# Kernel tuning notes

Measured on AMD Instinct MI355X. Metric: run time of the kernel, lower is better.

Reference implementation:

```python
import jax, jax.numpy as jnp
import numpy as np

NUM_GROUPS = 4
KERNEL_SIZE = 3


def _conv1x1(x, w, b):
    # x: [B,Cin,H,W], w: [Cout,Cin], b: [Cout]
    return jnp.einsum('bchw,oc->bohw', x, w) + b[None, :, None, None]


def _unfold(t, ks):
    # t: [B,G,Gd,H,W] -> patches [B,G,Gd,ks*ks,H,W] with zero padding (pad=ks//2)
    pad = ks // 2
    H, W = t.shape[-2:]
    tp = jnp.pad(t, ((0, 0), (0, 0), (0, 0), (pad, pad), (pad, pad)))
    return jnp.stack([tp[..., i:i + H, j:j + W]
                      for i in range(ks) for j in range(ks)], axis=3)


def setup_inputs() -> dict:
    key = jax.random.key(0)
    ks = jax.random.split(key, 7)
    B, Cin, C, H, W = 4, 256, 256, 64, 64
    s = 1.0 / np.sqrt(Cin)
    return {
        'x': jax.random.normal(ks[0], (B, Cin, H, W), dtype=jnp.float32),
        'wq': jax.random.normal(ks[1], (C, Cin), dtype=jnp.float32) * s,
        'bq': jax.random.normal(ks[2], (C,), dtype=jnp.float32) * 0.01,
        'wk': jax.random.normal(ks[3], (C, Cin), dtype=jnp.float32) * s,
        'bk': jax.random.normal(ks[4], (C,), dtype=jnp.float32) * 0.01,
        'wv': jax.random.normal(ks[5], (C, Cin), dtype=jnp.float32) * s,
        'bv': jax.random.normal(ks[6], (C,), dtype=jnp.float32) * 0.01,
    }


def reference(x, wq, bq, wk, bk, wv, bv):
    B, _, H, W = x.shape
    C = wq.shape[0]
    G = NUM_GROUPS
    Gd = C // G
    q = _conv1x1(x, wq, bq).reshape(B, G, Gd, H, W)
    k = _conv1x1(x, wk, bk).reshape(B, G, Gd, H, W)
    v = _conv1x1(x, wv, bv).reshape(B, G, Gd, H, W)
    kp = _unfold(k, KERNEL_SIZE)  # [B,G,Gd,k2,H,W]
    vp = _unfold(v, KERNEL_SIZE)  # [B,G,Gd,k2,H,W]
    attn = jnp.einsum('bgdhw,bgdphw->bgphw', q, kp)  # [B,G,k2,H,W]
    attn = jax.nn.softmax(attn, axis=2)
    out = jnp.einsum('bgphw,bgdphw->bgdhw', attn, vp)  # [B,G,Gd,H,W]
    return out.reshape(B, C, H, W)
```

## Files before the change

kernel.cpp:

```cpp
#include <hip/hip_runtime.h>
#include <cstddef>
#include <cstdint>

#define BDIM 4
#define HH   64
#define WW   64
#define HWSZ 4096
#define CIN  256

typedef __attribute__((ext_vector_type(4))) float f32x4;
typedef _Float16 f16x4_t __attribute__((ext_vector_type(4)));
typedef _Float16 f16x8_t __attribute__((ext_vector_type(8)));

__device__ __forceinline__ void lds_load16(const void* g, void* l) {
    __builtin_amdgcn_global_load_lds(
        (const __attribute__((address_space(1))) unsigned int*)g,
        (__attribute__((address_space(3))) unsigned int*)l, 16, 0, 0);
}

__global__ __launch_bounds__(512, 2) void fused_kernel(
    const float* __restrict__ x,
    const float* __restrict__ wq, const float* __restrict__ bq,
    const float* __restrict__ wk, const float* __restrict__ bk,
    const float* __restrict__ wv, const float* __restrict__ bv,
    float* __restrict__ out)
{
    __shared__ float    As[128 * 32];
    __shared__ float    Bs[32 * 384];
    __shared__ _Float16 qlds[256 * 64];
    __shared__ _Float16 klds[384 * 64];

    const int t   = threadIdx.x;
    const int bx0 = blockIdx.x;
    const int bx  = (bx0 & 7) * 32 + (bx0 >> 3);
    const int g   = bx & 3;
    const int ht  = (bx >> 2) & 15;
    const int b   = bx >> 6;
    const int h0  = ht * 4;

    const int l    = t & 63;
    const int wid  = t >> 6;
    const int lrow = l & 15;
    const int grp  = l >> 4;
    const int grp4 = grp * 4;
    const int wmA  = wid >> 2;
    const int wnA  = wid & 3;

    const float* xb = x + (size_t)b * CIN * HWSZ;

    const int ms  = t >> 3;
    const int kbs = ((t & 7) ^ (ms & 7)) * 4;
    const float* aSrcQ = wq + (size_t)(g * 64 + ms) * CIN + kbs;
    const float* aSrcK = wk + (size_t)(g * 64 + ms) * CIN + kbs;
    const float* aSrcV = wv + (size_t)(g * 64 + ms) * CIN + kbs;

    const float* bSrc[6];
    #pragma unroll
    for (int i = 0; i < 6; ++i) {
        const unsigned U = i * 512 + t;
        const unsigned k = U / 96u;
        const unsigned rem = U - k * 96u;
        const int r  = (int)(rem >> 4);
        const int u0 = (int)(rem & 15);
        int srow = h0 - 1 + r;
        srow = srow < 0 ? 0 : (srow > 63 ? 63 : srow);
        const int cu = u0 ^ (((int)(k >> 3)) << 2);
        bSrc[i] = xb + (size_t)k * HWSZ + srow * 64 + cu * 4;
    }

    const float* biasA = wmA ? bk : bq;
    f32x4 accA[4][6];
    #pragma unroll
    for (int mi = 0; mi < 4; ++mi) {
        const f32x4 bb = *(const f32x4*)&biasA[g * 64 + mi * 16 + grp4];
        #pragma unroll
        for (int ni = 0; ni < 6; ++ni) accA[mi][ni] = bb;
    }

    for (int kt = 0; kt < 8; ++kt) {
        const size_t ko = (size_t)kt * 32;
        lds_load16(aSrcQ + ko, As + t * 4);
        lds_load16(aSrcK + ko, As + 2048 + t * 4);
        #pragma unroll
        for (int i = 0; i < 6; ++i)
            lds_load16(bSrc[i] + ko * HWSZ, Bs + (i * 512 + t) * 4);
        __syncthreads();

        f16x8_t af[4];
        #pragma unroll
        for (int mi = 0; mi < 4; ++mi) {
            const int m = wmA * 64 + mi * 16 + lrow;
            const int s = m & 7;
            const f32x4 a0 = *(const f32x4*)&As[m * 32 + ((2 * grp) ^ s) * 4];
            const f32x4 a1 = *(const f32x4*)&As[m * 32 + ((2 * grp + 1) ^ s) * 4];
            f16x8_t f;
            #pragma unroll
            for (int j = 0; j < 4; ++j) { f[j] = (_Float16)a0[j]; f[4 + j] = (_Float16)a1[j]; }
            af[mi] = f;
        }
        f16x8_t bf[6];
        #pragma unroll
        for (int ni = 0; ni < 6; ++ni) {
            const int px  = wnA * 96 + ni * 16 + lrow;
            const int fo  = ((px >> 2) ^ (grp << 2)) * 4 + (px & 3);
            f16x8_t f;
            #pragma unroll
            for (int j = 0; j < 8; ++j) f[j] = (_Float16)Bs[(grp * 8 + j) * 384 + fo];
            bf[ni] = f;
        }
        #pragma unroll
        for (int mi = 0; mi < 4; ++mi)
            #pragma unroll
            for (int ni = 0; ni < 6; ++ni)
                accA[mi][ni] = __builtin_amdgcn_mfma_f32_16x16x32_f16(
                    af[mi], bf[ni], accA[mi][ni], 0, 0, 0);
        __syncthreads();
    }

    #pragma unroll
    for (int ni = 0; ni < 6; ++ni) {
        const int px = wnA * 96 + ni * 16 + lrow;
        const int spx = (wmA == 0) ? (px - 64) : px;
        const bool ok = (wmA == 0) ? (spx >= 0 && spx < 256) : true;
        _Float16* dl = (wmA == 0) ? qlds : klds;
        #pragma unroll
        for (int mi = 0; mi < 4; ++mi) {
            if (ok) {
                const int cb  = mi * 2 + (grp >> 1);
                const int off = (grp & 1) * 4;
                f16x4_t hv;
                #pragma unroll
                for (int j = 0; j < 4; ++j) hv[j] = (_Float16)accA[mi][ni][j];
                *(f16x4_t*)&dl[spx * 64 + ((cb ^ (spx & 7)) * 8) + off] = hv;
            }
        }
    }
    __syncthreads();

    const int pxi  = wid * 32 + (l & 31);
    const int chh  = l >> 5;
    const int hq   = h0 + (pxi >> 6);
    const int wcol = pxi & 63;

    float qf[32];
    #pragma unroll
    for (int jj = 0; jj < 4; ++jj) {
        const int cb = chh * 4 + jj;
        const f16x8_t qv = *(const f16x8_t*)&qlds[pxi * 64 + ((cb ^ (pxi & 7)) * 8)];
        #pragma unroll
        for (int e = 0; e < 8; ++e) qf[jj * 8 + e] = (float)qv[e];
    }

    float lg[9];
    #pragma unroll
    for (int p = 0; p < 9; ++p) {
        const int dh = p / 3 - 1, dw = p % 3 - 1;
        const int h2 = hq + dh, w2 = wcol + dw;
        float part = 0.f;
        if (h2 >= 0 && h2 < HH && w2 >= 0 && w2 < WW) {
            const int hpx = pxi + 64 + dh * 64 + dw;
            #pragma unroll
            for (int jj = 0; jj < 4; ++jj) {
                const int cb = chh * 4 + jj;
                const f16x8_t kv = *(const f16x8_t*)&klds[hpx * 64 + ((cb ^ (hpx & 7)) * 8)];
                #pragma unroll
                for (int e = 0; e < 8; ++e) part += qf[jj * 8 + e] * (float)kv[e];
            }
        }
        part += __shfl_xor(part, 32, 64);
        lg[p] = part;
    }

    float mx = lg[0];
    #pragma unroll
    for (int p = 1; p < 9; ++p) mx = fmaxf(mx, lg[p]);
    float a[9];
    float sum = 0.f;
    #pragma unroll
    for (int p = 0; p < 9; ++p) { a[p] = __expf(lg[p] - mx); sum += a[p]; }
    const float inv = 1.f / sum;
    #pragma unroll
    for (int p = 0; p < 9; ++p) a[p] *= inv;

    f32x4 accB[4][3];
    #pragma unroll
    for (int mi = 0; mi < 4; ++mi) {
        const f32x4 bb = *(const f32x4*)&bv[g * 64 + mi * 16 + grp4];
        #pragma unroll
        for (int ni = 0; ni < 3; ++ni) accB[mi][ni] = bb;
    }

    for (int kt = 0; kt < 8; ++kt) {
        const size_t ko = (size_t)kt * 32;
        lds_load16(aSrcV + ko, As + t * 4);
        #pragma unroll
        for (int i = 0; i < 6; ++i)
            lds_load16(bSrc[i] + ko * HWSZ, Bs + (i * 512 + t) * 4);
        __syncthreads();

        f16x8_t af[4];
        #pragma unroll
        for (int mi = 0; mi < 4; ++mi) {
            const int m = mi * 16 + lrow;
            const int s = m & 7;
            const f32x4 a0 = *(const f32x4*)&As[m * 32 + ((2 * grp) ^ s) * 4];
            const f32x4 a1 = *(const f32x4*)&As[m * 32 + ((2 * grp + 1) ^ s) * 4];
            f16x8_t f;
            #pragma unroll
            for (int j = 0; j < 4; ++j) { f[j] = (_Float16)a0[j]; f[4 + j] = (_Float16)a1[j]; }
            af[mi] = f;
        }
        f16x8_t bf[3];
        #pragma unroll
        for (int ni = 0; ni < 3; ++ni) {
            const int px = wid * 48 + ni * 16 + lrow;
            const int fo = ((px >> 2) ^ (grp << 2)) * 4 + (px & 3);
            f16x8_t f;
            #pragma unroll
            for (int j = 0; j < 8; ++j) f[j] = (_Float16)Bs[(grp * 8 + j) * 384 + fo];
            bf[ni] = f;
        }
        #pragma unroll
        for (int mi = 0; mi < 4; ++mi)
            #pragma unroll
            for (int ni = 0; ni < 3; ++ni)
                accB[mi][ni] = __builtin_amdgcn_mfma_f32_16x16x32_f16(
                    af[mi], bf[ni], accB[mi][ni], 0, 0, 0);
        __syncthreads();
    }

    #pragma unroll
    for (int ni = 0; ni < 3; ++ni) {
        const int px = wid * 48 + ni * 16 + lrow;
        #pragma unroll
        for (int mi = 0; mi < 4; ++mi) {
            const int cb  = mi * 2 + (grp >> 1);
            const int off = (grp & 1) * 4;
            f16x4_t hv;
            #pragma unroll
            for (int j = 0; j < 4; ++j) hv[j] = (_Float16)accB[mi][ni][j];
            *(f16x4_t*)&klds[px * 64 + ((cb ^ (px & 7)) * 8) + off] = hv;
        }
    }
    __syncthreads();

    float oacc[32];
    #pragma unroll
    for (int c = 0; c < 32; ++c) oacc[c] = 0.f;
    #pragma unroll
    for (int p = 0; p < 9; ++p) {
        const int dh = p / 3 - 1, dw = p % 3 - 1;
        const int h2 = hq + dh, w2 = wcol + dw;
        if (h2 < 0 || h2 >= HH || w2 < 0 || w2 >= WW) continue;
        const float ap = a[p];
        const int hpx = pxi + 64 + dh * 64 + dw;
        #pragma unroll
        for (int jj = 0; jj < 4; ++jj) {
            const int cb = chh * 4 + jj;
            const f16x8_t vv = *(const f16x8_t*)&klds[hpx * 64 + ((cb ^ (hpx & 7)) * 8)];
            #pragma unroll
            for (int e = 0; e < 8; ++e) oacc[jj * 8 + e] += ap * (float)vv[e];
        }
    }

    float* ob = out + ((size_t)(b * 256 + g * 64 + chh * 32)) * HWSZ + ht * 256 + pxi;
    #pragma unroll
    for (int c = 0; c < 32; ++c) ob[(size_t)c * HWSZ] = oacc[c];
}

extern "C" void kernel_launch(void* const* d_in, const int* in_sizes, int n_in,
                              void* d_out, int out_size, void* d_ws, size_t ws_size,
                              hipStream_t stream) {
    const float* x  = (const float*)d_in[0];
    const float* wq = (const float*)d_in[1];
    const float* bq = (const float*)d_in[2];
    const float* wk = (const float*)d_in[3];
    const float* bk = (const float*)d_in[4];
    const float* wv = (const float*)d_in[5];
    const float* bv = (const float*)d_in[6];
    float* out = (float*)d_out;

    fused_kernel<<<dim3(256), 512, 0, stream>>>(x, wq, bq, wk, bk, wv, bv, out);
}
```

Baseline: 37.54 us.

## Halve row tile, stage fp16 operands in LDS, aliased shared memory

Shrinks each block's spatial tile from 4 to 2 image rows, doubling the grid to 512 blocks. Global loads now go through registers and are converted to fp16 once before the LDS store, replacing the async global-to-LDS fp32 copies and their per-read conversions. Shared memory is packed into one aliased buffer so more blocks fit per CU, and launch bounds ask for 4 blocks. The cost is a larger share of halo rows recomputed for K/V (4 rows loaded per 2 output rows) and loads that are no longer asynchronous.

```diff
diff --git a/kernel.cpp b/kernel.cpp
--- a/kernel.cpp
+++ b/kernel.cpp
@@ -1,8 +1,6 @@
 #include <hip/hip_runtime.h>
 #include <cstddef>
-#include <cstdint>
-
-#define BDIM 4
+
 #define HH   64
 #define WW   64
 #define HWSZ 4096
@@ -12,143 +10,131 @@
 typedef _Float16 f16x4_t __attribute__((ext_vector_type(4)));
 typedef _Float16 f16x8_t __attribute__((ext_vector_type(8)));
 
-__device__ __forceinline__ void lds_load16(const void* g, void* l) {
-    __builtin_amdgcn_global_load_lds(
-        (const __attribute__((address_space(1))) unsigned int*)g,
-        (__attribute__((address_space(3))) unsigned int*)l, 16, 0, 0);
-}
-
-__global__ __launch_bounds__(512, 2) void fused_kernel(
+__global__ __launch_bounds__(512, 4) void fused_kernel(
     const float* __restrict__ x,
     const float* __restrict__ wq, const float* __restrict__ bq,
     const float* __restrict__ wk, const float* __restrict__ bk,
     const float* __restrict__ wv, const float* __restrict__ bv,
     float* __restrict__ out)
 {
-    __shared__ float    As[128 * 32];
-    __shared__ float    Bs[32 * 384];
-    __shared__ _Float16 qlds[256 * 64];
-    __shared__ _Float16 klds[384 * 64];
+    __shared__ __align__(16) char smem[57344];
+    _Float16* As   = (_Float16*)smem;
+    _Float16* Bs   = (_Float16*)(smem + 8192);
+    _Float16* qlds = (_Float16*)smem;
+    _Float16* klds = (_Float16*)(smem + 24576);
 
     const int t   = threadIdx.x;
     const int bx0 = blockIdx.x;
-    const int bx  = (bx0 & 7) * 32 + (bx0 >> 3);
+    const int bx  = (bx0 & 7) * 64 + (bx0 >> 3);
     const int g   = bx & 3;
-    const int ht  = (bx >> 2) & 15;
-    const int b   = bx >> 6;
-    const int h0  = ht * 4;
-
-    const int l    = t & 63;
-    const int wid  = t >> 6;
-    const int lrow = l & 15;
-    const int grp  = l >> 4;
+    const int ht  = (bx >> 2) & 31;
+    const int b   = bx >> 7;
+    const int h0  = ht * 2;
+
+    const int l    = t & 63, wid = t >> 6;
+    const int lrow = l & 15, grp = l >> 4;
     const int grp4 = grp * 4;
-    const int wmA  = wid >> 2;
-    const int wnA  = wid & 3;
+    const int swzr = (lrow >> 1) & 3;
+    const int wmA  = wid >> 2, wnA = wid & 3;
 
     const float* xb = x + (size_t)b * CIN * HWSZ;
 
-    const int ms  = t >> 3;
-    const int kbs = ((t & 7) ^ (ms & 7)) * 4;
-    const float* aSrcQ = wq + (size_t)(g * 64 + ms) * CIN + kbs;
-    const float* aSrcK = wk + (size_t)(g * 64 + ms) * CIN + kbs;
-    const float* aSrcV = wv + (size_t)(g * 64 + ms) * CIN + kbs;
-
-    const float* bSrc[6];
-    #pragma unroll
-    for (int i = 0; i < 6; ++i) {
-        const unsigned U = i * 512 + t;
-        const unsigned k = U / 96u;
-        const unsigned rem = U - k * 96u;
-        const int r  = (int)(rem >> 4);
-        const int u0 = (int)(rem & 15);
-        int srow = h0 - 1 + r;
-        srow = srow < 0 ? 0 : (srow > 63 ? 63 : srow);
-        const int cu = u0 ^ (((int)(k >> 3)) << 2);
-        bSrc[i] = xb + (size_t)k * HWSZ + srow * 64 + cu * 4;
-    }
+    const int smA = t >> 2, skA = t & 3;
+    const float* aqk = (smA < 64 ? wq + (size_t)(g * 64 + smA) * CIN
+                                 : wk + (size_t)(g * 64 + smA - 64) * CIN) + skA * 8;
+    const int awz = smA * 32 + ((skA ^ ((smA >> 1) & 3)) << 3);
+
+    const int mv = (t >> 2) & 63;
+    const float* avv = wv + (size_t)(g * 64 + mv) * CIN + skA * 8;
+    const int awzV = mv * 32 + ((skA ^ ((mv >> 1) & 3)) << 3);
+
+    const int spx0 = t & 127, skB = t >> 7;
+    const int spx1 = spx0 + 128;
+    int sr0 = h0 - 1 + (spx0 >> 6); sr0 = sr0 < 0 ? 0 : sr0;
+    int sr1 = h0 - 1 + (spx1 >> 6); sr1 = sr1 > 63 ? 63 : sr1;
+    const float* bgp0 = xb + (size_t)(skB * 8) * HWSZ + sr0 * 64 + (spx0 & 63);
+    const float* bgp1 = xb + (size_t)(skB * 8) * HWSZ + sr1 * 64 + (spx1 & 63);
+    const int bwz0 = spx0 * 32 + ((skB ^ ((spx0 >> 1) & 3)) << 3);
+    const int bwz1 = spx1 * 32 + ((skB ^ ((spx1 >> 1) & 3)) << 3);
 
     const float* biasA = wmA ? bk : bq;
-    f32x4 accA[4][6];
+    f32x4 accA[4][4];
     #pragma unroll
     for (int mi = 0; mi < 4; ++mi) {
         const f32x4 bb = *(const f32x4*)&biasA[g * 64 + mi * 16 + grp4];
         #pragma unroll
-        for (int ni = 0; ni < 6; ++ni) accA[mi][ni] = bb;
+        for (int ni = 0; ni < 4; ++ni) accA[mi][ni] = bb;
     }
 
     for (int kt = 0; kt < 8; ++kt) {
-        const size_t ko = (size_t)kt * 32;
-        lds_load16(aSrcQ + ko, As + t * 4);
-        lds_load16(aSrcK + ko, As + 2048 + t * 4);
-        #pragma unroll
-        for (int i = 0; i < 6; ++i)
-            lds_load16(bSrc[i] + ko * HWSZ, Bs + (i * 512 + t) * 4);
-        __syncthreads();
-
-        f16x8_t af[4];
-        #pragma unroll
-        for (int mi = 0; mi < 4; ++mi) {
-            const int m = wmA * 64 + mi * 16 + lrow;
-            const int s = m & 7;
-            const f32x4 a0 = *(const f32x4*)&As[m * 32 + ((2 * grp) ^ s) * 4];
-            const f32x4 a1 = *(const f32x4*)&As[m * 32 + ((2 * grp + 1) ^ s) * 4];
-            f16x8_t f;
-            #pragma unroll
-            for (int j = 0; j < 4; ++j) { f[j] = (_Float16)a0[j]; f[4 + j] = (_Float16)a1[j]; }
-            af[mi] = f;
-        }
-        f16x8_t bf[6];
-        #pragma unroll
-        for (int ni = 0; ni < 6; ++ni) {
-            const int px  = wnA * 96 + ni * 16 + lrow;
-            const int fo  = ((px >> 2) ^ (grp << 2)) * 4 + (px & 3);
-            f16x8_t f;
-            #pragma unroll
-            for (int j = 0; j < 8; ++j) f[j] = (_Float16)Bs[(grp * 8 + j) * 384 + fo];
-            bf[ni] = f;
-        }
-        #pragma unroll
-        for (int mi = 0; mi < 4; ++mi)
-            #pragma unroll
-            for (int ni = 0; ni < 6; ++ni)
+        const float4 A0 = *(const float4*)(aqk + kt * 32);
+        const float4 A1 = *(const float4*)(aqk + kt * 32 + 4);
+        float lb0[8], lb1[8];
+        #pragma unroll
+        for (int j = 0; j < 8; ++j) lb0[j] = bgp0[(size_t)(kt * 32 + j) * HWSZ];
+        #pragma unroll
+        for (int j = 0; j < 8; ++j) lb1[j] = bgp1[(size_t)(kt * 32 + j) * HWSZ];
+        __syncthreads();
+
+        f16x8_t fa, f0, f1;
+        const float* pA0 = (const float*)&A0;
+        const float* pA1 = (const float*)&A1;
+        #pragma unroll
+        for (int j = 0; j < 4; ++j) { fa[j] = (_Float16)pA0[j]; fa[4 + j] = (_Float16)pA1[j]; }
+        #pragma unroll
+        for (int j = 0; j < 8; ++j) { f0[j] = (_Float16)lb0[j]; f1[j] = (_Float16)lb1[j]; }
+        *(f16x8_t*)&As[awz]  = fa;
+        *(f16x8_t*)&Bs[bwz0] = f0;
+        *(f16x8_t*)&Bs[bwz1] = f1;
+        __syncthreads();
+
+        f16x8_t af[4], bf[4];
+        #pragma unroll
+        for (int mi = 0; mi < 4; ++mi)
+            af[mi] = *(const f16x8_t*)&As[(wmA * 64 + mi * 16 + lrow) * 32 + ((grp ^ swzr) << 3)];
+        #pragma unroll
+        for (int ni = 0; ni < 4; ++ni)
+            bf[ni] = *(const f16x8_t*)&Bs[(wnA * 64 + ni * 16 + lrow) * 32 + ((grp ^ swzr) << 3)];
+        #pragma unroll
+        for (int mi = 0; mi < 4; ++mi)
+            #pragma unroll
+            for (int ni = 0; ni < 4; ++ni)
                 accA[mi][ni] = __builtin_amdgcn_mfma_f32_16x16x32_f16(
                     af[mi], bf[ni], accA[mi][ni], 0, 0, 0);
-        __syncthreads();
-    }
-
-    #pragma unroll
-    for (int ni = 0; ni < 6; ++ni) {
-        const int px = wnA * 96 + ni * 16 + lrow;
-        const int spx = (wmA == 0) ? (px - 64) : px;
-        const bool ok = (wmA == 0) ? (spx >= 0 && spx < 256) : true;
-        _Float16* dl = (wmA == 0) ? qlds : klds;
+    }
+    __syncthreads();
+
+    #pragma unroll
+    for (int ni = 0; ni < 4; ++ni) {
+        const int px  = wnA * 64 + ni * 16 + lrow;
+        const int spx = px - 64;
         #pragma unroll
         for (int mi = 0; mi < 4; ++mi) {
-            if (ok) {
-                const int cb  = mi * 2 + (grp >> 1);
-                const int off = (grp & 1) * 4;
-                f16x4_t hv;
-                #pragma unroll
-                for (int j = 0; j < 4; ++j) hv[j] = (_Float16)accA[mi][ni][j];
-                *(f16x4_t*)&dl[spx * 64 + ((cb ^ (spx & 7)) * 8) + off] = hv;
+            f16x4_t hv;
+            #pragma unroll
+            for (int j = 0; j < 4; ++j) hv[j] = (_Float16)accA[mi][ni][j];
+            const int cb = mi * 2 + (grp >> 1), off = (grp & 1) * 4;
+            if (wmA == 0) {
+                if (spx >= 0 && spx < 128)
+                    *(f16x4_t*)&qlds[spx * 64 + ((cb ^ (spx & 7)) << 3) + off] = hv;
+            } else {
+                *(f16x4_t*)&klds[px * 64 + ((cb ^ (px & 7)) << 3) + off] = hv;
             }
         }
     }
     __syncthreads();
 
-    const int pxi  = wid * 32 + (l & 31);
-    const int chh  = l >> 5;
+    const int pxi  = wid * 16 + lrow;
+    const int cq   = grp;
     const int hq   = h0 + (pxi >> 6);
     const int wcol = pxi & 63;
 
-    float qf[32];
-    #pragma unroll
-    for (int jj = 0; jj < 4; ++jj) {
-        const int cb = chh * 4 + jj;
-        const f16x8_t qv = *(const f16x8_t*)&qlds[pxi * 64 + ((cb ^ (pxi & 7)) * 8)];
-        #pragma unroll
-        for (int e = 0; e < 8; ++e) qf[jj * 8 + e] = (float)qv[e];
+    float qf[16];
+    #pragma unroll
+    for (int hh2 = 0; hh2 < 2; ++hh2) {
+        const f16x8_t qv = *(const f16x8_t*)&qlds[pxi * 64 + (((2 * cq + hh2) ^ (pxi & 7)) << 3)];
+        #pragma unroll
+        for (int e = 0; e < 8; ++e) qf[hh2 * 8 + e] = (float)qv[e];
     }
 
     float lg[9];
@@ -160,13 +146,13 @@
         if (h2 >= 0 && h2 < HH && w2 >= 0 && w2 < WW) {
             const int hpx = pxi + 64 + dh * 64 + dw;
             #pragma unroll
-            for (int jj = 0; jj < 4; ++jj) {
-                const int cb = chh * 4 + jj;
-                const f16x8_t kv = *(const f16x8_t*)&klds[hpx * 64 + ((cb ^ (hpx & 7)) * 8)];
+            for (int hh2 = 0; hh2 < 2; ++hh2) {
+                const f16x8_t kv = *(const f16x8_t*)&klds[hpx * 64 + (((2 * cq + hh2) ^ (hpx & 7)) << 3)];
                 #pragma unroll
-                for (int e = 0; e < 8; ++e) part += qf[jj * 8 + e] * (float)kv[e];
+                for (int e = 0; e < 8; ++e) part += qf[hh2 * 8 + e] * (float)kv[e];
             }
         }
+        part += __shfl_xor(part, 16, 64);
         part += __shfl_xor(part, 32, 64);
         lg[p] = part;
     }
@@ -181,72 +167,75 @@
     const float inv = 1.f / sum;
     #pragma unroll
     for (int p = 0; p < 9; ++p) a[p] *= inv;
-
-    f32x4 accB[4][3];
+    __syncthreads();
+
+    f32x4 accB[4][2];
     #pragma unroll
     for (int mi = 0; mi < 4; ++mi) {
         const f32x4 bb = *(const f32x4*)&bv[g * 64 + mi * 16 + grp4];
-        #pragma unroll
-        for (int ni = 0; ni < 3; ++ni) accB[mi][ni] = bb;
+        accB[mi][0] = bb; accB[mi][1] = bb;
     }
 
     for (int kt = 0; kt < 8; ++kt) {
-        const size_t ko = (size_t)kt * 32;
-        lds_load16(aSrcV + ko, As + t * 4);
-        #pragma unroll
-        for (int i = 0; i < 6; ++i)
-            lds_load16(bSrc[i] + ko * HWSZ, Bs + (i * 512 + t) * 4);
-        __syncthreads();
-
-        f16x8_t af[4];
+        float4 V0, V1;
+        if (t < 256) {
+            V0 = *(const float4*)(avv + kt * 32);
+            V1 = *(const float4*)(avv + kt * 32 + 4);
+        }
+        float lb0[8], lb1[8];
+        #pragma unroll
+        for (int j = 0; j < 8; ++j) lb0[j] = bgp0[(size_t)(kt * 32 + j) * HWSZ];
+        #pragma unroll
+        for (int j = 0; j < 8; ++j) lb1[j] = bgp1[(size_t)(kt * 32 + j) * HWSZ];
+        __syncthreads();
+
+        if (t < 256) {
+            f16x8_t fv;
+            const float* pV0 = (const float*)&V0;
+            const float* pV1 = (const float*)&V1;
+            #pragma unroll
+            for (int j = 0; j < 4; ++j) { fv[j] = (_Float16)pV0[j]; fv[4 + j] = (_Float16)pV1[j]; }
+            *(f16x8_t*)&As[awzV] = fv;
+        }
+        f16x8_t f0, f1;
+        #pragma unroll
+        for (int j = 0; j < 8; ++j) { f0[j] = (_Float16)lb0[j]; f1[j] = (_Float16)lb1[j]; }
+        *(f16x8_t*)&Bs[bwz0] = f0;
+        *(f16x8_t*)&Bs[bwz1] = f1;
+        __syncthreads();
+
+        f16x8_t af[4], bf2[2];
+        #pragma unroll
+        for (int mi = 0; mi < 4; ++mi)
+            af[mi] = *(const f16x8_t*)&As[(mi * 16 + lrow) * 32 + ((grp ^ swzr) << 3)];
+        #pragma unroll
+        for (int ni = 0; ni < 2; ++ni)
+            bf2[ni] = *(const f16x8_t*)&Bs[(wid * 32 + ni * 16 + lrow) * 32 + ((grp ^ swzr) << 3)];
+        #pragma unroll
+        for (int mi = 0; mi < 4; ++mi)
+            #pragma unroll
+            for (int ni = 0; ni < 2; ++ni)
+                accB[mi][ni] = __builtin_amdgcn_mfma_f32_16x16x32_f16(
+                    af[mi], bf2[ni], accB[mi][ni], 0, 0, 0);
+    }
+
+    #pragma unroll
+    for (int ni = 0; ni < 2; ++ni) {
+        const int px = wid * 32 + ni * 16 + lrow;
         #pragma unroll
         for (int mi = 0; mi < 4; ++mi) {
-            const int m = mi * 16 + lrow;
-            const int s = m & 7;
-            const f32x4 a0 = *(const f32x4*)&As[m * 32 + ((2 * grp) ^ s) * 4];
-            const f32x4 a1 = *(const f32x4*)&As[m * 32 + ((2 * grp + 1) ^ s) * 4];
-            f16x8_t f;
-            #pragma unroll
-            for (int j = 0; j < 4; ++j) { f[j] = (_Float16)a0[j]; f[4 + j] = (_Float16)a1[j]; }
-            af[mi] = f;
-        }
-        f16x8_t bf[3];
-        #pragma unroll
-        for (int ni = 0; ni < 3; ++ni) {
-            const int px = wid * 48 + ni * 16 + lrow;
-            const int fo = ((px >> 2) ^ (grp << 2)) * 4 + (px & 3);
-            f16x8_t f;
-            #pragma unroll
-            for (int j = 0; j < 8; ++j) f[j] = (_Float16)Bs[(grp * 8 + j) * 384 + fo];
-            bf[ni] = f;
-        }
-        #pragma unroll
-        for (int mi = 0; mi < 4; ++mi)
-            #pragma unroll
-            for (int ni = 0; ni < 3; ++ni)
-                accB[mi][ni] = __builtin_amdgcn_mfma_f32_16x16x32_f16(
-                    af[mi], bf[ni], accB[mi][ni], 0, 0, 0);
-        __syncthreads();
-    }
-
-    #pragma unroll
-    for (int ni = 0; ni < 3; ++ni) {
-        const int px = wid * 48 + ni * 16 + lrow;
-        #pragma unroll
-        for (int mi = 0; mi < 4; ++mi) {
-            const int cb  = mi * 2 + (grp >> 1);
-            const int off = (grp & 1) * 4;
             f16x4_t hv;
             #pragma unroll
             for (int j = 0; j < 4; ++j) hv[j] = (_Float16)accB[mi][ni][j];
-            *(f16x4_t*)&klds[px * 64 + ((cb ^ (px & 7)) * 8) + off] = hv;
-        }
-    }
-    __syncthreads();
-
-    float oacc[32];
-    #pragma unroll
-    for (int c = 0; c < 32; ++c) oacc[c] = 0.f;
+            const int cb = mi * 2 + (grp >> 1), off = (grp & 1) * 4;
+            *(f16x4_t*)&klds[px * 64 + ((cb ^ (px & 7)) << 3) + off] = hv;
+        }
+    }
+    __syncthreads();
+
+    float oacc[16];
+    #pragma unroll
+    for (int c = 0; c < 16; ++c) oacc[c] = 0.f;
     #pragma unroll
     for (int p = 0; p < 9; ++p) {
         const int dh = p / 3 - 1, dw = p % 3 - 1;
@@ -255,17 +244,16 @@
         const float ap = a[p];
         const int hpx = pxi + 64 + dh * 64 + dw;
         #pragma unroll
-        for (int jj = 0; jj < 4; ++jj) {
-            const int cb = chh * 4 + jj;
-            const f16x8_t vv = *(const f16x8_t*)&klds[hpx * 64 + ((cb ^ (hpx & 7)) * 8)];
-            #pragma unroll
-            for (int e = 0; e < 8; ++e) oacc[jj * 8 + e] += ap * (float)vv[e];
-        }
-    }
-
-    float* ob = out + ((size_t)(b * 256 + g * 64 + chh * 32)) * HWSZ + ht * 256 + pxi;
-    #pragma unroll
-    for (int c = 0; c < 32; ++c) ob[(size_t)c * HWSZ] = oacc[c];
+        for (int hh2 = 0; hh2 < 2; ++hh2) {
+            const f16x8_t vv = *(const f16x8_t*)&klds[hpx * 64 + (((2 * cq + hh2) ^ (hpx & 7)) << 3)];
+            #pragma unroll
+            for (int e = 0; e < 8; ++e) oacc[hh2 * 8 + e] += ap * (float)vv[e];
+        }
+    }
+
+    float* ob = out + ((size_t)(b * 256 + g * 64 + cq * 16)) * HWSZ + h0 * 64 + pxi;
+    #pragma unroll
+    for (int c = 0; c < 16; ++c) ob[(size_t)c * HWSZ] = oacc[c];
 }
 
 extern "C" void kernel_launch(void* const* d_in, const int* in_sizes, int n_in,
@@ -280,5 +268,5 @@
     const float* bv = (const float*)d_in[6];
     float* out = (float*)d_out;
 
-    fused_kernel<<<dim3(256), 512, 0, stream>>>(x, wq, bq, wk, bk, wv, bv, out);
+    fused_kernel<<<dim3(512), 512, 0, stream>>>(x, wq, bq, wk, bk, wv, bv, out);
 }
```

After: 38.03 us. No clear change (+1.3%).
